# Kernel optimization log

Hardware: AMD Instinct MI355X
Metric: run time of the kernel (lower is better)

Reference implementation:

```python
import jax, jax.numpy as jnp
import numpy as np

# ---- module constants (from init_kwargs) ----
L = 16            # num_levels
T = 524288        # table_size (power of 2 -> uint32 wraparound-safe mod)
DIN = 3
FPL = 2           # FEATURES_PER_LEVEL
GRID_MIN, GRID_MAX = -1.0, 1.0
B = 262144

RES = jnp.asarray(np.exp(np.linspace(np.log(16.0), np.log(2048.0), L)), dtype=jnp.float32)  # (L,)
PRIMES = jnp.array([1, 2654435761, 805459861], dtype=jnp.uint32)                            # (3,)
# offsets match torch: format(i, '03b') -> MSB first
OFFSETS = jnp.array([[(i >> (DIN - 1 - d)) & 1 for d in range(DIN)] for i in range(2 ** DIN)], dtype=jnp.uint32)  # (8,3)
OFF_F = OFFSETS.astype(jnp.float32)
OFF_HASH = (OFFSETS * PRIMES).sum(-1)  # (8,) uint32; hash is linear in coords so corner offsets separate out


def setup_inputs() -> dict:
    key = jax.random.key(0)
    ks = jax.random.split(key, 8)
    return {
        "x": jax.random.uniform(ks[0], (B, DIN), jnp.float32, minval=GRID_MIN, maxval=GRID_MAX),
        "embeddings": jax.random.uniform(ks[1], (L, T, FPL), jnp.float32, minval=-1e-4, maxval=1e-4),
        "W1": jax.random.normal(ks[2], (64, L * FPL), jnp.float32) * (1.0 / np.sqrt(L * FPL)),
        "b1": jax.random.normal(ks[3], (64,), jnp.float32) * 0.01,
        "W2": jax.random.normal(ks[4], (64, 64), jnp.float32) * (1.0 / 8.0),
        "b2": jax.random.normal(ks[5], (64,), jnp.float32) * 0.01,
        "Wout": jax.random.normal(ks[6], (1, 64), jnp.float32) * (1.0 / 8.0),
        "bout": jax.random.normal(ks[7], (1,), jnp.float32) * 0.01,
    }


def reference(x, embeddings, W1, b1, W2, b2, Wout, bout):
    n = x.shape[0]
    x_norm = (x - GRID_MIN) / (GRID_MAX - GRID_MIN)          # (B,3) in [0,1)
    x_grid = x_norm[None, :, :] * RES[:, None, None]          # (L,B,3)
    x0 = jnp.floor(x_grid)
    w = x_grid - x0                                           # (L,B,3) fractional part
    # hashed = ((x0+offset) . primes) % T ; linear -> split base + offset hash (uint32 wrap == low bits of int64)
    base = (x0.astype(jnp.uint32) * PRIMES).sum(-1)           # (L,B)
    hashed = ((base[:, :, None] + OFF_HASH) % T).astype(jnp.int32)   # (L,B,8)
    corners = jnp.take_along_axis(
        embeddings, hashed.reshape(L, -1, 1), axis=1
    ).reshape(L, n, 2 ** DIN, FPL)                            # (L,B,8,2)
    # trilinear weights: prod over dims of (1-off) + w*(2*off-1)
    per_dim = 1.0 - OFF_F + w[:, :, None, :] * (2.0 * OFF_F - 1.0)   # (L,B,8,3)
    cw = per_dim.prod(-1)                                     # (L,B,8)
    value = jnp.einsum('lbc,lbcf->lbf', cw, corners)          # (L,B,2)
    encoded = jnp.moveaxis(value, 0, 1).reshape(n, L * FPL)   # (B,32)
    h = jax.nn.silu(encoded @ W1.T + b1)
    h = jax.nn.silu(h @ W2.T + b2)
    return (h @ Wout.T + bout).squeeze(-1)                    # (B,)
```

## Files before the change

### kernel.cpp

```cpp
#include <hip/hip_runtime.h>
#include <math.h>
#include <stdint.h>

#define NLEV 16
#define TBL 524288
#define TMASK (TBL - 1)
#define BLOCK 256
#define SPT 4
#define P1 2654435761u
#define P2 805459861u

struct ResArr { float r[NLEV]; };

typedef __attribute__((ext_vector_type(4))) float f32x4;
typedef __attribute__((ext_vector_type(8))) short bf16x8;
struct __attribute__((packed, aligned(8))) f4wrap { f32x4 v; };

__device__ __forceinline__ float silu_f(float v) {
    return __fdividef(v, 1.0f + __expf(-v));
}

__device__ __forceinline__ uint32_t f2bf(float f) {
    uint32_t u = __float_as_uint(f);
    return (u + 0x7FFFu + ((u >> 16) & 1u)) >> 16;
}
__device__ __forceinline__ float bf2f(uint32_t b) {
    return __uint_as_float(b << 16);
}
__device__ __forceinline__ void split_bf(float x, bf16x8& hi, bf16x8& lo, int e) {
    const uint32_t hb = f2bf(x);
    hi[e] = (short)hb;
    lo[e] = (short)f2bf(x - bf2f(hb));
}

__global__ void __launch_bounds__(BLOCK)
encode_kernel(const float* __restrict__ x,
              const float* __restrict__ emb,
              float2* __restrict__ enc_ws,
              int nsamp, ResArr res)
{
    const int bid  = blockIdx.x;
    const int half = gridDim.x >> 1;
    int lvl, chunk;
    if (bid < half) { lvl = bid & 7;               chunk = bid >> 3; }
    else            { lvl = 8 + ((bid - half) & 7); chunk = (bid - half) >> 3; }

    const int t  = threadIdx.x;
    const int s0 = chunk * (BLOCK * SPT) + t;
    const float rs = res.r[lvl];
    const float* tabf = emb + (size_t)lvl * TBL * 2;

    uint32_t i0[SPT][4];
    float w0[SPT], w1[SPT], w2[SPT];
    uint32_t bad = 0;

    #pragma unroll
    for (int p = 0; p < SPT; ++p) {
        const int s = s0 + p * BLOCK;
        const float xv0 = __builtin_nontemporal_load(&x[(size_t)s * 3 + 0]);
        const float xv1 = __builtin_nontemporal_load(&x[(size_t)s * 3 + 1]);
        const float xv2 = __builtin_nontemporal_load(&x[(size_t)s * 3 + 2]);
        const float g0 = (xv0 + 1.0f) * 0.5f * rs;
        const float g1 = (xv1 + 1.0f) * 0.5f * rs;
        const float g2 = (xv2 + 1.0f) * 0.5f * rs;
        const float f0 = floorf(g0), f1 = floorf(g1), f2 = floorf(g2);
        w0[p] = g0 - f0; w1[p] = g1 - f1; w2[p] = g2 - f2;
        const uint32_t hb = (uint32_t)f0 + (uint32_t)f1 * P1 + (uint32_t)f2 * P2;
        #pragma unroll
        for (int q = 0; q < 4; ++q) {
            uint32_t h = hb;
            if ((q >> 1) & 1) h += P1;
            if (q & 1)        h += P2;
            i0[p][q] = h & TMASK;
            bad |= (uint32_t)(i0[p][q] == TMASK);
        }
    }

    f32x4 v[SPT][4];
    if (__builtin_expect(__any((int)bad), 0)) {
        #pragma unroll
        for (int p = 0; p < SPT; ++p)
            #pragma unroll
            for (int q = 0; q < 4; ++q) {
                const uint32_t a = i0[p][q];
                const uint32_t b = (a + 1u) & TMASK;
                const float2 lo = *(const float2*)(tabf + 2 * (size_t)a);
                const float2 hi = *(const float2*)(tabf + 2 * (size_t)b);
                v[p][q] = f32x4{lo.x, lo.y, hi.x, hi.y};
            }
    } else {
        #pragma unroll
        for (int p = 0; p < SPT; ++p)
            #pragma unroll
            for (int q = 0; q < 4; ++q)
                v[p][q] = ((const f4wrap*)(tabf + 2 * (size_t)i0[p][q]))->v;
    }

    #pragma unroll
    for (int p = 0; p < SPT; ++p) {
        const float om0 = 1.0f - w0[p], om1 = 1.0f - w1[p], om2 = 1.0f - w2[p];
        float e0 = 0.0f, e1 = 0.0f;
        #pragma unroll
        for (int q = 0; q < 4; ++q) {
            float wb = (((q >> 1) & 1) ? w1[p] : om1) * ((q & 1) ? w2[p] : om2);
            const float c0 = om0 * wb;
            const float c1 = w0[p] * wb;
            e0 = fmaf(c0, v[p][q].x, fmaf(c1, v[p][q].z, e0));
            e1 = fmaf(c0, v[p][q].y, fmaf(c1, v[p][q].w, e1));
        }
        const int s = s0 + p * BLOCK;
        union { float2 f; unsigned long long u; } pk;
        pk.f.x = e0; pk.f.y = e1;
        __builtin_nontemporal_store(pk.u,
            (unsigned long long*)&enc_ws[(size_t)lvl * nsamp + s]);
    }
}

__global__ void __launch_bounds__(BLOCK)
mlp_mfma_kernel(const float2* __restrict__ enc_ws,
                const float* __restrict__ W1,
                const float* __restrict__ b1,
                const float* __restrict__ W2,
                const float* __restrict__ b2,
                const float* __restrict__ Wout,
                const float* __restrict__ bout,
                float* __restrict__ out, int nsamp)
{
    __shared__ __align__(16) float hbuf[4][32 * 68];

    const int tid  = threadIdx.x;
    const int wid  = tid >> 6;
    const int lane = tid & 63;
    const int l15  = lane & 15;
    const int g    = lane >> 4;
    const int sbase = blockIdx.x * 128 + wid * 32;
    float* hw = hbuf[wid];

    bf16x8 b1hi[4], b1lo[4];
    float  b1v[4];
    #pragma unroll
    for (int n = 0; n < 4; ++n) {
        const float* wr = W1 + (n * 16 + l15) * 32 + g * 8;
        const f32x4 wv0 = ((const f4wrap*)wr)->v;
        const f32x4 wv1 = ((const f4wrap*)(wr + 4))->v;
        #pragma unroll
        for (int e = 0; e < 4; ++e) {
            split_bf(wv0[e], b1hi[n], b1lo[n], e);
            split_bf(wv1[e], b1hi[n], b1lo[n], e + 4);
        }
        b1v[n] = b1[n * 16 + l15];
    }

    #pragma unroll
    for (int m = 0; m < 2; ++m) {
        bf16x8 ahi, alo;
        const int s = sbase + m * 16 + l15;
        #pragma unroll
        for (int d = 0; d < 4; ++d) {
            union { unsigned long long u; float f[2]; } uv;
            uv.u = *(const unsigned long long*)&enc_ws[(size_t)(g * 4 + d) * nsamp + s];
            split_bf(uv.f[0], ahi, alo, 2 * d);
            split_bf(uv.f[1], ahi, alo, 2 * d + 1);
        }
        #pragma unroll
        for (int n = 0; n < 4; ++n) {
            f32x4 acc = {0.f, 0.f, 0.f, 0.f};
            acc = __builtin_amdgcn_mfma_f32_16x16x32_bf16(alo, b1hi[n], acc, 0, 0, 0);
            acc = __builtin_amdgcn_mfma_f32_16x16x32_bf16(ahi, b1lo[n], acc, 0, 0, 0);
            acc = __builtin_amdgcn_mfma_f32_16x16x32_bf16(ahi, b1hi[n], acc, 0, 0, 0);
            #pragma unroll
            for (int r = 0; r < 4; ++r) {
                const int row = m * 16 + g * 4 + r;
                const int col = n * 16 + l15;
                hw[row * 68 + col] = silu_f(acc[r] + b1v[n]);
            }
        }
    }

    f32x4 acc2[2][4];
    #pragma unroll
    for (int m = 0; m < 2; ++m)
        #pragma unroll
        for (int n = 0; n < 4; ++n)
            acc2[m][n] = f32x4{0.f, 0.f, 0.f, 0.f};

    #pragma unroll
    for (int ks = 0; ks < 2; ++ks) {
        bf16x8 b2hi[4], b2lo[4];
        #pragma unroll
        for (int n = 0; n < 4; ++n) {
            const float* wr = W2 + (n * 16 + l15) * 64 + ks * 32 + g * 8;
            const f32x4 wv0 = ((const f4wrap*)wr)->v;
            const f32x4 wv1 = ((const f4wrap*)(wr + 4))->v;
            #pragma unroll
            for (int e = 0; e < 4; ++e) {
                split_bf(wv0[e], b2hi[n], b2lo[n], e);
                split_bf(wv1[e], b2hi[n], b2lo[n], e + 4);
            }
        }
        #pragma unroll
        for (int m = 0; m < 2; ++m) {
            bf16x8 ahi, alo;
            const float* hr = &hw[(m * 16 + l15) * 68 + ks * 32 + g * 8];
            const f32x4 h0 = *(const f32x4*)hr;
            const f32x4 h1 = *(const f32x4*)(hr + 4);
            #pragma unroll
            for (int e = 0; e < 4; ++e) {
                split_bf(h0[e], ahi, alo, e);
                split_bf(h1[e], ahi, alo, e + 4);
            }
            #pragma unroll
            for (int n = 0; n < 4; ++n) {
                acc2[m][n] = __builtin_amdgcn_mfma_f32_16x16x32_bf16(alo, b2hi[n], acc2[m][n], 0, 0, 0);
                acc2[m][n] = __builtin_amdgcn_mfma_f32_16x16x32_bf16(ahi, b2lo[n], acc2[m][n], 0, 0, 0);
                acc2[m][n] = __builtin_amdgcn_mfma_f32_16x16x32_bf16(ahi, b2hi[n], acc2[m][n], 0, 0, 0);
            }
        }
    }

    float b2v[4], wov[4];
    #pragma unroll
    for (int n = 0; n < 4; ++n) {
        b2v[n] = b2[n * 16 + l15];
        wov[n] = Wout[n * 16 + l15];
    }
    const float bo = bout[0];

    #pragma unroll
    for (int m = 0; m < 2; ++m) {
        float part[4] = {0.f, 0.f, 0.f, 0.f};
        #pragma unroll
        for (int n = 0; n < 4; ++n)
            #pragma unroll
            for (int r = 0; r < 4; ++r)
                part[r] += silu_f(acc2[m][n][r] + b2v[n]) * wov[n];
        #pragma unroll
        for (int mask = 1; mask <= 8; mask <<= 1)
            #pragma unroll
            for (int r = 0; r < 4; ++r)
                part[r] += __shfl_xor(part[r], mask, 64);
        if (l15 == 0) {
            #pragma unroll
            for (int r = 0; r < 4; ++r)
                out[sbase + m * 16 + g * 4 + r] = part[r] + bo;
        }
    }
}

__global__ void __launch_bounds__(BLOCK)
hashgrid_mlp_kernel(const float* __restrict__ x,
                    const float* __restrict__ emb,
                    const float* __restrict__ W1,
                    const float* __restrict__ b1,
                    const float* __restrict__ W2,
                    const float* __restrict__ b2,
                    const float* __restrict__ Wout,
                    const float* __restrict__ bout,
                    float* __restrict__ out,
                    ResArr res)
{
    const int t = threadIdx.x;
    const int s = blockIdx.x * BLOCK + t;

    const float xn0 = (x[(size_t)s * 3 + 0] + 1.0f) * 0.5f;
    const float xn1 = (x[(size_t)s * 3 + 1] + 1.0f) * 0.5f;
    const float xn2 = (x[(size_t)s * 3 + 2] + 1.0f) * 0.5f;

    float enc[2 * NLEV];
    #pragma unroll
    for (int l = 0; l < NLEV; ++l) {
        const float rs = res.r[l];
        const float g0 = xn0 * rs, g1 = xn1 * rs, g2 = xn2 * rs;
        const float f0 = floorf(g0), f1 = floorf(g1), f2 = floorf(g2);
        const float w0 = g0 - f0, w1 = g1 - f1, w2 = g2 - f2;
        const uint32_t hb = (uint32_t)f0 + (uint32_t)f1 * P1 + (uint32_t)f2 * P2;
        const float2* tab = (const float2*)emb + (size_t)l * TBL;
        const float om0 = 1.0f - w0, om1 = 1.0f - w1, om2 = 1.0f - w2;
        float e0 = 0.0f, e1 = 0.0f;
        #pragma unroll
        for (int c = 0; c < 8; ++c) {
            const uint32_t cb0 = (c >> 2) & 1, cb1 = (c >> 1) & 1, cb2 = c & 1;
            uint32_t h = hb;
            if (cb0) h += 1u;
            if (cb1) h += P1;
            if (cb2) h += P2;
            h &= TMASK;
            const float2 vv = tab[h];
            float wt = (cb0 ? w0 : om0) * (cb1 ? w1 : om1);
            wt *= (cb2 ? w2 : om2);
            e0 = fmaf(wt, vv.x, e0);
            e1 = fmaf(wt, vv.y, e1);
        }
        enc[2 * l + 0] = e0;
        enc[2 * l + 1] = e1;
    }

    float h1[64];
    #pragma unroll
    for (int i = 0; i < 64; ++i) {
        float acc = b1[i];
        #pragma unroll
        for (int k = 0; k < 32; ++k)
            acc = fmaf(enc[k], W1[i * 32 + k], acc);
        h1[i] = silu_f(acc);
    }
    float o = bout[0];
    #pragma unroll
    for (int i = 0; i < 64; ++i) {
        float acc = b2[i];
        #pragma unroll
        for (int k = 0; k < 64; ++k)
            acc = fmaf(h1[k], W2[i * 64 + k], acc);
        o = fmaf(silu_f(acc), Wout[i], o);
    }
    out[s] = o;
}

extern "C" void kernel_launch(void* const* d_in, const int* in_sizes, int n_in,
                              void* d_out, int out_size, void* d_ws, size_t ws_size,
                              hipStream_t stream) {
    const float* x    = (const float*)d_in[0];
    const float* emb  = (const float*)d_in[1];
    const float* W1   = (const float*)d_in[2];
    const float* b1   = (const float*)d_in[3];
    const float* W2   = (const float*)d_in[4];
    const float* b2   = (const float*)d_in[5];
    const float* Wout = (const float*)d_in[6];
    const float* bout = (const float*)d_in[7];
    float* out = (float*)d_out;

    ResArr res;
    const double lg0 = log(16.0), lg1 = log(2048.0);
    for (int i = 0; i < NLEV; ++i)
        res.r[i] = (float)exp(lg0 + (lg1 - lg0) * (double)i / 15.0);

    const int n = in_sizes[0] / 3;
    const size_t ws_needed = (size_t)n * NLEV * sizeof(float2);

    if (ws_size >= ws_needed) {
        float2* enc_ws = (float2*)d_ws;
        const int chunks = n / (BLOCK * SPT);
        dim3 gridA(2 * 8 * chunks);
        encode_kernel<<<gridA, BLOCK, 0, stream>>>(x, emb, enc_ws, n, res);
        dim3 gridB(n / 128);
        mlp_mfma_kernel<<<gridB, BLOCK, 0, stream>>>(enc_ws, W1, b1, W2, b2,
                                                     Wout, bout, out, n);
    } else {
        dim3 grid(n / BLOCK);
        hashgrid_mlp_kernel<<<grid, BLOCK, 0, stream>>>(x, emb, W1, b1, W2, b2,
                                                        Wout, bout, out, res);
    }
}
```

Baseline: 137.8 us.

## Store encoded features and hidden activations as bf16 and drop low-part MFMAs

The encode kernel now packs its two per-level features into one bf16 pair instead of a float2, which halves the workspace written and later read by the MLP kernel. The MLP kernel loads these bf16 values straight into MFMA operands. It also keeps the layer-1 activations in shared memory as bf16, removing the hi/lo split of activations and one of the three MFMAs per tile in both layers. Weights keep their hi/lo split, but activations lose precision to plain bf16, so the output error against the fp32 reference goes up.

```diff
diff --git a/kernel.cpp b/kernel.cpp
--- a/kernel.cpp
+++ b/kernel.cpp
@@ -36,7 +36,7 @@
 __global__ void __launch_bounds__(BLOCK)
 encode_kernel(const float* __restrict__ x,
               const float* __restrict__ emb,
-              float2* __restrict__ enc_ws,
+              uint32_t* __restrict__ enc_ws,
               int nsamp, ResArr res)
 {
     const int bid  = blockIdx.x;
@@ -109,15 +109,13 @@
             e1 = fmaf(c0, v[p][q].y, fmaf(c1, v[p][q].w, e1));
         }
         const int s = s0 + p * BLOCK;
-        union { float2 f; unsigned long long u; } pk;
-        pk.f.x = e0; pk.f.y = e1;
-        __builtin_nontemporal_store(pk.u,
-            (unsigned long long*)&enc_ws[(size_t)lvl * nsamp + s]);
+        const uint32_t pk = f2bf(e0) | (f2bf(e1) << 16);
+        __builtin_nontemporal_store(pk, &enc_ws[(size_t)lvl * nsamp + s]);
     }
 }
 
 __global__ void __launch_bounds__(BLOCK)
-mlp_mfma_kernel(const float2* __restrict__ enc_ws,
+mlp_mfma_kernel(const uint32_t* __restrict__ enc_ws,
                 const float* __restrict__ W1,
                 const float* __restrict__ b1,
                 const float* __restrict__ W2,
@@ -126,7 +124,7 @@
                 const float* __restrict__ bout,
                 float* __restrict__ out, int nsamp)
 {
-    __shared__ __align__(16) float hbuf[4][32 * 68];
+    __shared__ __align__(16) unsigned short hbuf[4][32 * 72];
 
     const int tid  = threadIdx.x;
     const int wid  = tid >> 6;
@@ -134,7 +132,7 @@
     const int l15  = lane & 15;
     const int g    = lane >> 4;
     const int sbase = blockIdx.x * 128 + wid * 32;
-    float* hw = hbuf[wid];
+    unsigned short* hw = hbuf[wid];
 
     bf16x8 b1hi[4], b1lo[4];
     float  b1v[4];
@@ -153,26 +151,21 @@
 
     #pragma unroll
     for (int m = 0; m < 2; ++m) {
-        bf16x8 ahi, alo;
+        union { uint32_t u[4]; bf16x8 v; } af;
         const int s = sbase + m * 16 + l15;
         #pragma unroll
-        for (int d = 0; d < 4; ++d) {
-            union { unsigned long long u; float f[2]; } uv;
-            uv.u = *(const unsigned long long*)&enc_ws[(size_t)(g * 4 + d) * nsamp + s];
-            split_bf(uv.f[0], ahi, alo, 2 * d);
-            split_bf(uv.f[1], ahi, alo, 2 * d + 1);
-        }
+        for (int d = 0; d < 4; ++d)
+            af.u[d] = enc_ws[(size_t)(g * 4 + d) * nsamp + s];
         #pragma unroll
         for (int n = 0; n < 4; ++n) {
             f32x4 acc = {0.f, 0.f, 0.f, 0.f};
-            acc = __builtin_amdgcn_mfma_f32_16x16x32_bf16(alo, b1hi[n], acc, 0, 0, 0);
-            acc = __builtin_amdgcn_mfma_f32_16x16x32_bf16(ahi, b1lo[n], acc, 0, 0, 0);
-            acc = __builtin_amdgcn_mfma_f32_16x16x32_bf16(ahi, b1hi[n], acc, 0, 0, 0);
+            acc = __builtin_amdgcn_mfma_f32_16x16x32_bf16(af.v, b1lo[n], acc, 0, 0, 0);
+            acc = __builtin_amdgcn_mfma_f32_16x16x32_bf16(af.v, b1hi[n], acc, 0, 0, 0);
             #pragma unroll
             for (int r = 0; r < 4; ++r) {
                 const int row = m * 16 + g * 4 + r;
                 const int col = n * 16 + l15;
-                hw[row * 68 + col] = silu_f(acc[r] + b1v[n]);
+                hw[row * 72 + col] = (unsigned short)f2bf(silu_f(acc[r] + b1v[n]));
             }
         }
     }
@@ -200,20 +193,11 @@
         }
         #pragma unroll
         for (int m = 0; m < 2; ++m) {
-            bf16x8 ahi, alo;
-            const float* hr = &hw[(m * 16 + l15) * 68 + ks * 32 + g * 8];
-            const f32x4 h0 = *(const f32x4*)hr;
-            const f32x4 h1 = *(const f32x4*)(hr + 4);
-            #pragma unroll
-            for (int e = 0; e < 4; ++e) {
-                split_bf(h0[e], ahi, alo, e);
-                split_bf(h1[e], ahi, alo, e + 4);
-            }
+            const bf16x8 a2 = *(const bf16x8*)&hw[(m * 16 + l15) * 72 + ks * 32 + g * 8];
             #pragma unroll
             for (int n = 0; n < 4; ++n) {
-                acc2[m][n] = __builtin_amdgcn_mfma_f32_16x16x32_bf16(alo, b2hi[n], acc2[m][n], 0, 0, 0);
-                acc2[m][n] = __builtin_amdgcn_mfma_f32_16x16x32_bf16(ahi, b2lo[n], acc2[m][n], 0, 0, 0);
-                acc2[m][n] = __builtin_amdgcn_mfma_f32_16x16x32_bf16(ahi, b2hi[n], acc2[m][n], 0, 0, 0);
+                acc2[m][n] = __builtin_amdgcn_mfma_f32_16x16x32_bf16(a2, b2lo[n], acc2[m][n], 0, 0, 0);
+                acc2[m][n] = __builtin_amdgcn_mfma_f32_16x16x32_bf16(a2, b2hi[n], acc2[m][n], 0, 0, 0);
             }
         }
     }
@@ -335,10 +319,10 @@
         res.r[i] = (float)exp(lg0 + (lg1 - lg0) * (double)i / 15.0);
 
     const int n = in_sizes[0] / 3;
-    const size_t ws_needed = (size_t)n * NLEV * sizeof(float2);
+    const size_t ws_needed = (size_t)n * NLEV * sizeof(uint32_t);
 
     if (ws_size >= ws_needed) {
-        float2* enc_ws = (float2*)d_ws;
+        uint32_t* enc_ws = (uint32_t*)d_ws;
         const int chunks = n / (BLOCK * SPT);
         dim3 gridA(2 * 8 * chunks);
         encode_kernel<<<gridA, BLOCK, 0, stream>>>(x, emb, enc_ws, n, res);
```

New measurement: 131.9 us. 1.04x faster.
